# Performance work log

Measured on AMD Instinct MI355X. Metric: run time of the kernel, lower is better.

## Reference

```python
import jax, jax.numpy as jnp
import numpy as np

ELL = 10.0                 # init_ell (fixed, is_learning_kernel=False)
THRESH = 0.1               # min_correlation_threshold


def quat_to_rotmat(q):
    """pypose SO3 quaternion (x, y, z, w) -> [.., 3, 3] rotation matrix."""
    q = q / jnp.linalg.norm(q, axis=-1, keepdims=True)
    x, y, z, w = q[..., 0], q[..., 1], q[..., 2], q[..., 3]
    r00 = 1 - 2 * (y * y + z * z); r01 = 2 * (x * y - z * w); r02 = 2 * (x * z + y * w)
    r10 = 2 * (x * y + z * w); r11 = 1 - 2 * (x * x + z * z); r12 = 2 * (y * z - x * w)
    r20 = 2 * (x * z - y * w); r21 = 2 * (y * z + x * w); r22 = 1 - 2 * (x * x + y * y)
    return jnp.stack([jnp.stack([r00, r01, r02], -1),
                      jnp.stack([r10, r11, r12], -1),
                      jnp.stack([r20, r21, r22], -1)], -2)


def setup_inputs() -> dict:
    key = jax.random.key(0)
    k1, k2, k3, k4, k5 = jax.random.split(key, 5)
    B, N, C = 2, 4096, 32
    return {
        "pc1": jax.random.normal(k1, (B, 3, N), dtype=jnp.float32),
        "pc2": jax.random.normal(k2, (B, 3, N), dtype=jnp.float32),
        "x_feat": jax.random.normal(k3, (B, C, 3, N), dtype=jnp.float32),
        "y_feat": jax.random.normal(k4, (B, C, 3, N), dtype=jnp.float32),
        "T_quat": jax.random.normal(k5, (B, 4), dtype=jnp.float32),
    }


def reference(pc1, pc2, x_feat, y_feat, T_quat):
    # [B, C, 3, N] -> [B, N, C, 3]
    x = jnp.transpose(x_feat, (0, 3, 1, 2))
    y = jnp.transpose(y_feat, (0, 3, 1, 2))
    # [B, 3, N] -> [B, N, 1, 3]; prepend coords as an extra channel
    p1 = jnp.transpose(pc1, (0, 2, 1))[:, :, None, :]
    p2 = jnp.transpose(pc2, (0, 2, 1))[:, :, None, :]
    x = jnp.concatenate([p1, x], axis=2)   # [B, N, C+1, 3]
    y = jnp.concatenate([p2, y], axis=2)   # [B, M, C+1, 3]
    # rotate every 3-vector of y by the batch rotation
    R = quat_to_rotmat(T_quat)             # [B, 3, 3]
    y = jnp.einsum('bij,bmcj->bmci', R, y)
    B, N = x.shape[0], x.shape[1]
    D = x.shape[2] * x.shape[3]            # (C+1)*3
    xf = x.reshape(B, N, D)
    yf = y.reshape(B, -1, D)
    # RBF gram: exp(-||x_i - y_j||^2 / (2 ell^2)), via GEMM expansion
    sq = (jnp.sum(xf * xf, -1)[:, :, None]
          + jnp.sum(yf * yf, -1)[:, None, :]
          - 2.0 * jnp.einsum('bnd,bmd->bnm', xf, yf))
    gram = jnp.exp(-jnp.maximum(sq, 0.0) / (2.0 * ELL * ELL))
    gram = jnp.where(gram > THRESH, gram, jnp.zeros((), gram.dtype))
    ip_sum = jnp.sum(gram)
    return (ip_sum, gram)
```

## Files before the change

### kernel.cpp

```cpp
#include <hip/hip_runtime.h>
#include <hip/hip_bf16.h>

#define BB 2
#define NN 4096
#define CC 32
#define PG 16

typedef __attribute__((ext_vector_type(8))) short short8;
typedef __attribute__((ext_vector_type(4))) float f32x4;

struct __attribute__((aligned(4))) f4a { float a, b, c, d; };

__device__ __forceinline__ unsigned short f2bf(float v) {
    return __builtin_bit_cast(unsigned short, __float2bfloat16(v));
}

__device__ __forceinline__ size_t chunk_off(int b, int n16, int kb) {
    return (((size_t)b * 256 + n16) * 4 + kb) * 512;
}

__global__ __launch_bounds__(256) void prep_kernel(
    const float* __restrict__ pc1, const float* __restrict__ pc2,
    const float* __restrict__ xfeat, const float* __restrict__ yfeat,
    const float* __restrict__ quat,
    __hip_bfloat16* __restrict__ Xp, __hip_bfloat16* __restrict__ Yp,
    float* __restrict__ px, float* __restrict__ py)
{
    int idx = blockIdx.x * 256 + threadIdx.x;
    if (idx >= PG * BB * NN) return;
    int g = idx >> 13;
    int rem = idx & 8191;
    int b = rem >> 12;
    int n = rem & 4095;
    int k0 = g * 8;

    float qx = quat[b*4+0], qy = quat[b*4+1], qz = quat[b*4+2], qw = quat[b*4+3];
    float qi = rsqrtf(qx*qx + qy*qy + qz*qz + qw*qw);
    qx *= qi; qy *= qi; qz *= qi; qw *= qi;
    float r00 = 1.f-2.f*(qy*qy+qz*qz), r01 = 2.f*(qx*qy-qz*qw), r02 = 2.f*(qx*qz+qy*qw);
    float r10 = 2.f*(qx*qy+qz*qw), r11 = 1.f-2.f*(qx*qx+qz*qz), r12 = 2.f*(qy*qz-qx*qw);
    float r20 = 2.f*(qx*qz-qy*qw), r21 = 2.f*(qy*qz+qx*qw), r22 = 1.f-2.f*(qx*qx+qy*qy);

    unsigned short hx[8], hy[8];
    float sx = 0.f, sy = 0.f;
    #pragma unroll
    for (int t = 0; t < 8; ++t) {
        int k = k0 + t;
        float vx = 0.f, wy = 0.f;
        if (k < 99) {
            int c = k / 3, comp = k - 3*c;
            const float* xsrc = (c == 0)
                ? (pc1 + (size_t)(b*3 + comp) * NN)
                : (xfeat + ((size_t)(b*CC + c-1)*3 + comp) * NN);
            vx = xsrc[n];
            const float* ybase = (c == 0)
                ? (pc2 + (size_t)b*3*NN)
                : (yfeat + (size_t)(b*CC + c-1)*3*NN);
            float u0 = ybase[n], u1 = ybase[NN + n], u2 = ybase[2*NN + n];
            wy = (comp == 0) ? r00*u0 + r01*u1 + r02*u2
               : (comp == 1) ? r10*u0 + r11*u1 + r12*u2
                             : r20*u0 + r21*u1 + r22*u2;
        }
        sx += vx*vx; sy += wy*wy;
        hx[t] = f2bf(vx);
        hy[t] = f2bf(wy);
    }

    int kb = g >> 2, ks = g & 3;
    size_t off = chunk_off(b, n >> 4, kb) + (size_t)(ks*16 + (n & 15)) * 8;
    short8 vx8, vy8;
    #pragma unroll
    for (int t = 0; t < 8; ++t) { vx8[t] = (short)hx[t]; vy8[t] = (short)hy[t]; }
    *(short8*)(Xp + off) = vx8;
    *(short8*)(Yp + off) = vy8;

    int pidx = g * (BB*NN) + b*NN + n;
    px[pidx] = sx; py[pidx] = sy;
}

__global__ __launch_bounds__(256) void reduce_kernel(
    const float* __restrict__ px, const float* __restrict__ py,
    float* __restrict__ xn, float* __restrict__ yn, float* __restrict__ out)
{
    int i = blockIdx.x * 256 + threadIdx.x;
    if (i >= BB * NN) return;
    float sx = 0.f, sy = 0.f;
    #pragma unroll
    for (int g = 0; g < PG; ++g) { sx += px[g*(BB*NN) + i]; sy += py[g*(BB*NN) + i]; }
    xn[i] = sx; yn[i] = sy;
    if (i == 0) out[0] = 0.f;
}

__global__ __launch_bounds__(256) void gram_kernel(
    const __hip_bfloat16* __restrict__ Xp, const __hip_bfloat16* __restrict__ Yp,
    const float* __restrict__ xn, const float* __restrict__ yn,
    float* __restrict__ out)
{
    __shared__ float red[4];
    int bid = blockIdx.x;
    int work = (bid & 7) * 256 + (bid >> 3);
    int b  = work >> 10;
    int rem = work & 1023;
    int tN = rem >> 5;
    int tM = rem & 31;

    int tid = threadIdx.x;
    int wid = tid >> 6, lane = tid & 63;
    int wr = wid >> 1, wc = wid & 1;
    int q = lane >> 4, cl = lane & 15;

    f32x4 acc[4][4] = {};
    #pragma unroll
    for (int kb = 0; kb < 4; ++kb) {
        short8 yfr[4], xfr[4];
        #pragma unroll
        for (int i = 0; i < 4; ++i)
            yfr[i] = ((const short8*)(Yp + chunk_off(b, tM*8 + wc*4 + i, kb)))[lane];
        #pragma unroll
        for (int j = 0; j < 4; ++j)
            xfr[j] = ((const short8*)(Xp + chunk_off(b, tN*8 + wr*4 + j, kb)))[lane];
        #pragma unroll
        for (int i = 0; i < 4; ++i)
            #pragma unroll
            for (int j = 0; j < 4; ++j)
                acc[i][j] = __builtin_amdgcn_mfma_f32_16x16x32_bf16(
                    yfr[i], xfr[j], acc[i][j], 0, 0, 0);
    }

    int rowb = tN*128 + wr*64;
    int colb = tM*128 + wc*64;
    float lsum = 0.f;
    #pragma unroll
    for (int j = 0; j < 4; ++j) {
        int row = rowb + j*16 + cl;
        float xv = xn[b*NN + row];
        size_t obase = 1 + (size_t)(b*NN + row) * NN;
        #pragma unroll
        for (int i = 0; i < 4; ++i) {
            int col0 = colb + i*16 + q*4;
            f32x4 yv = *(const f32x4*)(yn + b*NN + col0);
            float g[4];
            #pragma unroll
            for (int r = 0; r < 4; ++r) {
                float sq = fmaxf(xv + yv[r] - 2.f * acc[i][j][r], 0.f);
                float e = __expf(-sq * 0.005f);
                g[r] = (e > 0.1f) ? e : 0.f;
                lsum += g[r];
            }
            f4a t; t.a = g[0]; t.b = g[1]; t.c = g[2]; t.d = g[3];
            *(f4a*)(out + obase + col0) = t;
        }
    }

    #pragma unroll
    for (int off = 32; off > 0; off >>= 1) lsum += __shfl_down(lsum, off, 64);
    if (lane == 0) red[wid] = lsum;
    __syncthreads();
    if (tid == 0) atomicAdd(out, red[0] + red[1] + red[2] + red[3]);
}

extern "C" void kernel_launch(void* const* d_in, const int* in_sizes, int n_in,
                              void* d_out, int out_size, void* d_ws, size_t ws_size,
                              hipStream_t stream) {
    const float* pc1   = (const float*)d_in[0];
    const float* pc2   = (const float*)d_in[1];
    const float* xfeat = (const float*)d_in[2];
    const float* yfeat = (const float*)d_in[3];
    const float* quat  = (const float*)d_in[4];
    float* out = (float*)d_out;

    __hip_bfloat16* Xp = (__hip_bfloat16*)d_ws;
    __hip_bfloat16* Yp = Xp + (size_t)BB * 256 * 4 * 512;
    float* xn = (float*)(Yp + (size_t)BB * 256 * 4 * 512);
    float* yn = xn + (size_t)BB * NN;
    float* px = yn + (size_t)BB * NN;
    float* py = px + (size_t)PG * BB * NN;

    prep_kernel<<<(PG*BB*NN + 255)/256, 256, 0, stream>>>(
        pc1, pc2, xfeat, yfeat, quat, Xp, Yp, px, py);
    reduce_kernel<<<(BB*NN + 255)/256, 256, 0, stream>>>(px, py, xn, yn, out);
    gram_kernel<<<2048, 256, 0, stream>>>(Xp, Yp, xn, yn, out);
}
```

Before: 179.1 us.

## Switch gram GEMM to 32x32x16 MFMA with matching operand layout

```diff
diff --git a/kernel.cpp b/kernel.cpp
--- a/kernel.cpp
+++ b/kernel.cpp
@@ -8,15 +8,14 @@
 
 typedef __attribute__((ext_vector_type(8))) short short8;
 typedef __attribute__((ext_vector_type(4))) float f32x4;
-
-struct __attribute__((aligned(4))) f4a { float a, b, c, d; };
+typedef __attribute__((ext_vector_type(16))) float f32x16;
 
 __device__ __forceinline__ unsigned short f2bf(float v) {
     return __builtin_bit_cast(unsigned short, __float2bfloat16(v));
 }
 
-__device__ __forceinline__ size_t chunk_off(int b, int n16, int kb) {
-    return (((size_t)b * 256 + n16) * 4 + kb) * 512;
+__device__ __forceinline__ size_t chunk_off(int b, int n32, int kb) {
+    return (((size_t)b * 128 + n32) * 8 + kb) * 512;
 }
 
 __global__ __launch_bounds__(256) void prep_kernel(
@@ -66,8 +65,7 @@
         hy[t] = f2bf(wy);
     }
 
-    int kb = g >> 2, ks = g & 3;
-    size_t off = chunk_off(b, n >> 4, kb) + (size_t)(ks*16 + (n & 15)) * 8;
+    size_t off = chunk_off(b, n >> 5, g >> 1) + (size_t)(((g & 1)*32 + (n & 31)) * 8);
     short8 vx8, vy8;
     #pragma unroll
     for (int t = 0; t < 8; ++t) { vx8[t] = (short)hx[t]; vy8[t] = (short)hy[t]; }
@@ -107,48 +105,51 @@
     int tid = threadIdx.x;
     int wid = tid >> 6, lane = tid & 63;
     int wr = wid >> 1, wc = wid & 1;
-    int q = lane >> 4, cl = lane & 15;
+    int cl = lane & 31, hl = lane >> 5;
 
-    f32x4 acc[4][4] = {};
+    f32x16 acc[2][2] = {};
     #pragma unroll
-    for (int kb = 0; kb < 4; ++kb) {
-        short8 yfr[4], xfr[4];
+    for (int kb = 0; kb < 8; ++kb) {
+        short8 xfr[2], yfr[2];
         #pragma unroll
-        for (int i = 0; i < 4; ++i)
-            yfr[i] = ((const short8*)(Yp + chunk_off(b, tM*8 + wc*4 + i, kb)))[lane];
+        for (int fi = 0; fi < 2; ++fi)
+            xfr[fi] = ((const short8*)(Xp + chunk_off(b, tN*4 + wr*2 + fi, kb)))[lane];
         #pragma unroll
-        for (int j = 0; j < 4; ++j)
-            xfr[j] = ((const short8*)(Xp + chunk_off(b, tN*8 + wr*4 + j, kb)))[lane];
+        for (int fj = 0; fj < 2; ++fj)
+            yfr[fj] = ((const short8*)(Yp + chunk_off(b, tM*4 + wc*2 + fj, kb)))[lane];
         #pragma unroll
-        for (int i = 0; i < 4; ++i)
+        for (int fi = 0; fi < 2; ++fi)
             #pragma unroll
-            for (int j = 0; j < 4; ++j)
-                acc[i][j] = __builtin_amdgcn_mfma_f32_16x16x32_bf16(
-                    yfr[i], xfr[j], acc[i][j], 0, 0, 0);
+            for (int fj = 0; fj < 2; ++fj)
+                acc[fi][fj] = __builtin_amdgcn_mfma_f32_32x32x16_bf16(
+                    xfr[fi], yfr[fj], acc[fi][fj], 0, 0, 0);
     }
 
-    int rowb = tN*128 + wr*64;
-    int colb = tM*128 + wc*64;
     float lsum = 0.f;
     #pragma unroll
-    for (int j = 0; j < 4; ++j) {
-        int row = rowb + j*16 + cl;
-        float xv = xn[b*NN + row];
-        size_t obase = 1 + (size_t)(b*NN + row) * NN;
+    for (int fi = 0; fi < 2; ++fi) {
+        int rbase = tN*128 + wr*64 + fi*32 + 4*hl;
+        f32x4 xq0 = *(const f32x4*)(xn + b*NN + rbase);
+        f32x4 xq1 = *(const f32x4*)(xn + b*NN + rbase + 8);
+        f32x4 xq2 = *(const f32x4*)(xn + b*NN + rbase + 16);
+        f32x4 xq3 = *(const f32x4*)(xn + b*NN + rbase + 24);
         #pragma unroll
-        for (int i = 0; i < 4; ++i) {
-            int col0 = colb + i*16 + q*4;
-            f32x4 yv = *(const f32x4*)(yn + b*NN + col0);
-            float g[4];
+        for (int fj = 0; fj < 2; ++fj) {
+            int col = tM*128 + wc*64 + fj*32 + cl;
+            float yv = yn[b*NN + col];
             #pragma unroll
-            for (int r = 0; r < 4; ++r) {
-                float sq = fmaxf(xv + yv[r] - 2.f * acc[i][j][r], 0.f);
+            for (int r = 0; r < 16; ++r) {
+                int grp = r >> 2, rr = (r & 3) + 8*grp;
+                float xv = (grp == 0) ? xq0[r & 3]
+                         : (grp == 1) ? xq1[r & 3]
+                         : (grp == 2) ? xq2[r & 3]
+                                      : xq3[r & 3];
+                float sq = fmaxf(xv + yv - 2.f * acc[fi][fj][r], 0.f);
                 float e = __expf(-sq * 0.005f);
-                g[r] = (e > 0.1f) ? e : 0.f;
-                lsum += g[r];
+                float g = (e > 0.1f) ? e : 0.f;
+                out[1 + (size_t)(b*NN + rbase + rr) * NN + col] = g;
+                lsum += g;
             }
-            f4a t; t.a = g[0]; t.b = g[1]; t.c = g[2]; t.d = g[3];
-            *(f4a*)(out + obase + col0) = t;
         }
     }
 
@@ -170,8 +171,8 @@
     float* out = (float*)d_out;
 
     __hip_bfloat16* Xp = (__hip_bfloat16*)d_ws;
-    __hip_bfloat16* Yp = Xp + (size_t)BB * 256 * 4 * 512;
-    float* xn = (float*)(Yp + (size_t)BB * 256 * 4 * 512);
+    __hip_bfloat16* Yp = Xp + (size_t)BB * 128 * 8 * 512;
+    float* xn = (float*)(Yp + (size_t)BB * 128 * 8 * 512);
     float* yn = xn + (size_t)BB * NN;
     float* px = yn + (size_t)BB * NN;
     float* py = px + (size_t)PG * BB * NN;
```

Result: no change. 181.4 us (+1.3%).
